# Kernel tuning notes

Hardware: AMD Instinct MI355X
Metric: run time of the kernel (lower is better)

## Reference

```python
import jax, jax.numpy as jnp
import numpy as np

B, T, D_Q, D_V, ATTN, FILTERS, KSIZE = 64, 2048, 1024, 512, 128, 32, 31


def setup_inputs() -> dict:
    key = jax.random.key(0)
    ks = jax.random.split(key, 10)
    query = jax.random.normal(ks[0], (B, D_Q), dtype=jnp.float32)
    values = jax.random.normal(ks[1], (B, T, D_V), dtype=jnp.float32)
    keys = jax.random.normal(ks[2], (B, T, ATTN), dtype=jnp.float32)
    state = jax.random.uniform(ks[3], (B, T), dtype=jnp.float32)
    # learned parameters
    W_q = jax.random.normal(ks[4], (D_Q, ATTN), dtype=jnp.float32) * 0.02
    conv_kernel = jax.random.normal(ks[5], (KSIZE, 1, FILTERS), dtype=jnp.float32) * 0.1  # (W, In, Out)
    conv_bias = jnp.zeros((FILTERS,), dtype=jnp.float32)
    W_loc = jax.random.normal(ks[6], (FILTERS, ATTN), dtype=jnp.float32) * 0.1
    v_att = jax.random.normal(ks[7], (ATTN, 1), dtype=jnp.float32) * 0.1
    att_bias = jax.random.normal(ks[8], (ATTN,), dtype=jnp.float32) * 0.02
    return {"query": query, "values": values, "keys": keys, "state": state,
            "W_q": W_q, "conv_kernel": conv_kernel, "conv_bias": conv_bias,
            "W_loc": W_loc, "v_att": v_att, "att_bias": att_bias}


def reference(query, values, keys, state, W_q, conv_kernel, conv_bias, W_loc, v_att, att_bias):
    # processed_query: [B, 1, ATTN]
    pq = (query @ W_q)[:, None, :]
    # location features: Conv1D same-padding over alignments [B, T, 1] -> [B, T, FILTERS]
    loc = jax.lax.conv_general_dilated(
        state[:, :, None], conv_kernel,
        window_strides=(1,), padding='SAME',
        dimension_numbers=('NWC', 'WIO', 'NWC')) + conv_bias
    ploc = loc @ W_loc                                  # [B, T, ATTN]
    score = jnp.tanh(keys + pq + ploc + att_bias) @ v_att  # [B, T, 1]
    alignment = jax.nn.softmax(score, axis=1)           # [B, T, 1]
    attention = jnp.sum(alignment * values, axis=1)     # [B, D_V]
    alignment = jnp.squeeze(alignment, axis=2)          # [B, T]
    attention_state = alignment + state                 # cumulate=True
    return (attention, alignment, attention_state)
```

## Files before the change

kernel.cpp:

```cpp
#include <hip/hip_runtime.h>
#include <hip/hip_bf16.h>

#define B 64
#define T 2048
#define D_Q 1024
#define D_V 512
#define ATTN 128
#define FILTERS 32
#define KSIZE 31

#define PQ_OFF 0
#define CW_OFF 8192
#define PB_OFF (8192 + 3968)
#define SC_OFF (8192 + 3968 + 128)
#define ML_OFF (SC_OFF + 131072)
#define PART_OFF (ML_OFF + 4096)

#define AT_OFF 0
#define AL_OFF 32768
#define ST_OFF (32768 + 131072)

__device__ __forceinline__ float tanh_fast(float x) {
    float e = __expf(2.f * x);
    return 1.f - 2.f / (e + 1.f);
}

__global__ void __launch_bounds__(256)
k1_precompute(const float* __restrict__ query,
              const float* __restrict__ Wq,
              const float* __restrict__ ck,
              const float* __restrict__ cbias,
              const float* __restrict__ Wl,
              const float* __restrict__ abias,
              float* __restrict__ ws) {
    int tid = threadIdx.x;
    if (blockIdx.x < B) {
        int b = blockIdx.x;
        int q = tid & 31;
        int s = tid >> 5;
        __shared__ __align__(16) float sq[D_Q];
        __shared__ float4 red[256];
        ((float4*)sq)[tid] = ((const float4*)(query + (size_t)b * D_Q))[tid];
        __syncthreads();

        const float4* Wq4 = (const float4*)Wq;
        float4 acc = make_float4(0.f, 0.f, 0.f, 0.f);
        int dbase = s << 7;
#pragma unroll 16
        for (int i = 0; i < 128; ++i) {
            int d = dbase + i;
            float sd = sq[d];
            float4 w = Wq4[(size_t)d * 32 + q];
            acc.x += sd * w.x; acc.y += sd * w.y;
            acc.z += sd * w.z; acc.w += sd * w.w;
        }
        red[tid] = acc;
        __syncthreads();
        if (tid < 128) {
            float4 o = red[tid + 128];
            acc = red[tid];
            acc.x += o.x; acc.y += o.y; acc.z += o.z; acc.w += o.w;
            red[tid] = acc;
        }
        __syncthreads();
        if (tid < 64) {
            float4 o = red[tid + 64];
            acc = red[tid];
            acc.x += o.x; acc.y += o.y; acc.z += o.z; acc.w += o.w;
            red[tid] = acc;
        }
        __syncthreads();
        if (tid < 32) {
            float4 o = red[tid + 32];
            acc = red[tid];
            acc.x += o.x; acc.y += o.y; acc.z += o.z; acc.w += o.w;
            ((float4*)(ws + PQ_OFF))[b * 32 + tid] = acc;
        }
    } else {
        __shared__ float swl[FILTERS * ATTN];
        for (int i = tid; i < FILTERS * ATTN; i += 256) swl[i] = Wl[i];
        __syncthreads();
        if (tid < ATTN) {
            int a = tid;
            for (int k = 0; k < KSIZE; ++k) {
                float acc = 0.f;
#pragma unroll
                for (int f = 0; f < FILTERS; ++f) acc += ck[k * FILTERS + f] * swl[f * ATTN + a];
                ws[CW_OFF + k * ATTN + a] = acc;
            }
            float pb = abias[a];
#pragma unroll
            for (int f = 0; f < FILTERS; ++f) pb += cbias[f] * swl[f * ATTN + a];
            ws[PB_OFF + a] = pb;
        }
    }
}

__global__ void __launch_bounds__(256)
k2_fused(const float* __restrict__ keys,
         const float* __restrict__ state,
         const float* __restrict__ values,
         const float* __restrict__ vatt,
         float* __restrict__ ws) {
    int bid = blockIdx.x;
    int b = bid >> 5;
    int c = bid & 31;
    int t0 = c << 6;
    int tid = threadIdx.x;
    int a = tid & 127;
    int h = tid >> 7;

    __shared__ __align__(16) float sstate[96];
    __shared__ float sred[128];
    __shared__ float sal[64];
    __shared__ float4 spart[128];

    if (tid < 96) {
        int idx = t0 + tid - 15;
        sstate[tid] = (idx >= 0 && idx < T) ? state[b * T + idx] : 0.f;
    }

    float cw[KSIZE];
#pragma unroll
    for (int k = 0; k < KSIZE; ++k) cw[k] = ws[CW_OFF + k * ATTN + a];
    float pqa = ws[PQ_OFF + b * ATTN + a] + ws[PB_OFF + a];
    float vat = vatt[a];

    __syncthreads();

    const float* keyrow = keys + ((size_t)b * T + t0) * ATTN + a;
    const float4* sv = (const float4*)sstate;

    for (int s4 = 0; s4 < 4; ++s4) {
        int ts = h * 32 + s4 * 8;
        float kv[8];
#pragma unroll
        for (int j = 0; j < 8; ++j) kv[j] = keyrow[(size_t)(ts + j) * ATTN];
        float w[40];
#pragma unroll
        for (int q = 0; q < 10; ++q) {
            float4 v = sv[(ts >> 2) + q];
            w[4 * q + 0] = v.x; w[4 * q + 1] = v.y;
            w[4 * q + 2] = v.z; w[4 * q + 3] = v.w;
        }
        float sc[8];
#pragma unroll
        for (int j = 0; j < 8; ++j) sc[j] = 0.f;
#pragma unroll
        for (int k = 0; k < KSIZE; ++k) {
#pragma unroll
            for (int j = 0; j < 8; ++j) sc[j] += w[j + k] * cw[k];
        }
#pragma unroll
        for (int j = 0; j < 8; ++j) {
            float x = kv[j] + pqa + sc[j];
            float cc = tanh_fast(x) * vat;
#pragma unroll
            for (int off = 32; off >= 1; off >>= 1) cc += __shfl_xor(cc, off);
            if ((tid & 63) == 0) sred[(ts + j) * 2 + (a >> 6)] = cc;
        }
    }
    __syncthreads();

    if (tid < 64) {
        float s = sred[tid * 2] + sred[tid * 2 + 1];
        ws[SC_OFF + b * T + t0 + tid] = s;
        float m = s;
#pragma unroll
        for (int off = 32; off >= 1; off >>= 1) m = fmaxf(m, __shfl_xor(m, off));
        float e = __expf(s - m);
        sal[tid] = e;
        float l = e;
#pragma unroll
        for (int off = 32; off >= 1; off >>= 1) l += __shfl_xor(l, off);
        if (tid == 0) {
            ws[ML_OFF + (b * 32 + c) * 2 + 0] = m;
            ws[ML_OFF + (b * 32 + c) * 2 + 1] = l;
        }
    }
    __syncthreads();

    int d4 = tid & 127;
    const float4* V = (const float4*)values + ((size_t)b * T + t0) * (D_V / 4) + d4;
    float4 acc = make_float4(0.f, 0.f, 0.f, 0.f);
#pragma unroll 8
    for (int i = 0; i < 32; ++i) {
        int tl = h * 32 + i;
        float al = sal[tl];
        float4 v = V[(size_t)tl * (D_V / 4)];
        acc.x += al * v.x; acc.y += al * v.y;
        acc.z += al * v.z; acc.w += al * v.w;
    }
    if (h == 1) spart[d4] = acc;
    __syncthreads();
    if (h == 0) {
        float4 o = spart[d4];
        acc.x += o.x; acc.y += o.y; acc.z += o.z; acc.w += o.w;
        ((float4*)(ws + PART_OFF))[(size_t)(b * 32 + c) * (D_V / 4) + d4] = acc;
    }
}

__global__ void __launch_bounds__(256)
k_combine(const float* __restrict__ state,
          const float* __restrict__ ws,
          float* __restrict__ out) {
    int b = blockIdx.x;
    int tid = threadIdx.x;
    __shared__ float sw[32];
    __shared__ float sM, sinvL;

    if (tid < 32) {
        float m = ws[ML_OFF + (b * 32 + tid) * 2 + 0];
        float l = ws[ML_OFF + (b * 32 + tid) * 2 + 1];
        float M = m;
#pragma unroll
        for (int off = 16; off >= 1; off >>= 1) M = fmaxf(M, __shfl_xor(M, off));
        float wgt = __expf(m - M);
        sw[tid] = wgt;
        float L = l * wgt;
#pragma unroll
        for (int off = 16; off >= 1; off >>= 1) L += __shfl_xor(L, off);
        if (tid == 0) { sM = M; sinvL = 1.f / L; }
    }
    __syncthreads();

    float M = sM, invL = sinvL;

#pragma unroll
    for (int r = 0; r < 2; ++r) {
        int d = tid + (r << 8);
        float acc = 0.f;
#pragma unroll 8
        for (int c = 0; c < 32; ++c)
            acc += sw[c] * ws[PART_OFF + (size_t)(b * 32 + c) * D_V + d];
        out[AT_OFF + b * D_V + d] = acc * invL;
    }

#pragma unroll
    for (int k = 0; k < 8; ++k) {
        int t = tid + (k << 8);
        float s = ws[SC_OFF + b * T + t];
        float al = __expf(s - M) * invL;
        out[AL_OFF + b * T + t] = al;
        out[ST_OFF + b * T + t] = al + state[b * T + t];
    }
}

extern "C" void kernel_launch(void* const* d_in, const int* in_sizes, int n_in,
                              void* d_out, int out_size, void* d_ws, size_t ws_size,
                              hipStream_t stream) {
    const float* query  = (const float*)d_in[0];
    const float* values = (const float*)d_in[1];
    const float* keys   = (const float*)d_in[2];
    const float* state  = (const float*)d_in[3];
    const float* Wq     = (const float*)d_in[4];
    const float* ck     = (const float*)d_in[5];
    const float* cbias  = (const float*)d_in[6];
    const float* Wl     = (const float*)d_in[7];
    const float* vatt   = (const float*)d_in[8];
    const float* abias  = (const float*)d_in[9];
    float* out = (float*)d_out;
    float* ws  = (float*)d_ws;

    k1_precompute<<<B + 1, 256, 0, stream>>>(query, Wq, ck, cbias, Wl, abias, ws);
    k2_fused<<<B * (T / 64), 256, 0, stream>>>(keys, state, values, vatt, ws);
    k_combine<<<B, 256, 0, stream>>>(state, ws, out);
}
```

Measured before the change: 432.7 us.

## Split fused score/value kernel into separate score and weighted-value kernels

The fused kernel is split in two. The first computes scores and per-chunk exp weights and writes the weights to workspace. The second reads those weights and does the weighted sum over values, with each half-block handling a 64-step chunk, so no shared-memory reduction is needed. The aim is to let each kernel run at better occupancy and keep register pressure from the conv path out of the value-streaming loop, at the cost of an extra launch and a workspace round trip.

```diff
diff --git a/kernel.cpp b/kernel.cpp
--- a/kernel.cpp
+++ b/kernel.cpp
@@ -15,6 +15,7 @@
 #define SC_OFF (8192 + 3968 + 128)
 #define ML_OFF (SC_OFF + 131072)
 #define PART_OFF (ML_OFF + 4096)
+#define SAL_OFF (PART_OFF + 1048576)
 
 #define AT_OFF 0
 #define AL_OFF 32768
@@ -85,7 +86,7 @@
             for (int k = 0; k < KSIZE; ++k) {
                 float acc = 0.f;
 #pragma unroll
-                for (int f = 0; f < FILTERS; ++f) acc += ck[k * FILTERS + f] * swl[f * ATTN + a];
+            for (int f = 0; f < FILTERS; ++f) acc += ck[k * FILTERS + f] * swl[f * ATTN + a];
                 ws[CW_OFF + k * ATTN + a] = acc;
             }
             float pb = abias[a];
@@ -97,11 +98,10 @@
 }
 
 __global__ void __launch_bounds__(256)
-k2_fused(const float* __restrict__ keys,
-         const float* __restrict__ state,
-         const float* __restrict__ values,
-         const float* __restrict__ vatt,
-         float* __restrict__ ws) {
+k2a_scores(const float* __restrict__ keys,
+           const float* __restrict__ state,
+           const float* __restrict__ vatt,
+           float* __restrict__ ws) {
     int bid = blockIdx.x;
     int b = bid >> 5;
     int c = bid & 31;
@@ -112,8 +112,6 @@
 
     __shared__ __align__(16) float sstate[96];
     __shared__ float sred[128];
-    __shared__ float sal[64];
-    __shared__ float4 spart[128];
 
     if (tid < 96) {
         int idx = t0 + tid - 15;
@@ -169,7 +167,7 @@
 #pragma unroll
         for (int off = 32; off >= 1; off >>= 1) m = fmaxf(m, __shfl_xor(m, off));
         float e = __expf(s - m);
-        sal[tid] = e;
+        ws[SAL_OFF + b * T + t0 + tid] = e;
         float l = e;
 #pragma unroll
         for (int off = 32; off >= 1; off >>= 1) l += __shfl_xor(l, off);
@@ -178,26 +176,36 @@
             ws[ML_OFF + (b * 32 + c) * 2 + 1] = l;
         }
     }
-    __syncthreads();
-
+}
+
+__global__ void __launch_bounds__(256)
+k2b_partial(const float* __restrict__ values,
+            float* __restrict__ ws) {
+    int bid = blockIdx.x;
+    int b = bid >> 4;
+    int cp = bid & 15;
+    int t0 = cp << 7;
+    int tid = threadIdx.x;
+    int h = tid >> 7;
     int d4 = tid & 127;
-    const float4* V = (const float4*)values + ((size_t)b * T + t0) * (D_V / 4) + d4;
+
+    __shared__ float sal[128];
+    if (tid < 128) sal[tid] = ws[SAL_OFF + b * T + t0 + tid];
+    __syncthreads();
+
+    const float4* V = (const float4*)values
+                      + ((size_t)b * T + t0 + (h << 6)) * (D_V / 4) + d4;
+    const float* wgt = sal + (h << 6);
     float4 acc = make_float4(0.f, 0.f, 0.f, 0.f);
-#pragma unroll 8
-    for (int i = 0; i < 32; ++i) {
-        int tl = h * 32 + i;
-        float al = sal[tl];
-        float4 v = V[(size_t)tl * (D_V / 4)];
+#pragma unroll 16
+    for (int i = 0; i < 64; ++i) {
+        float al = wgt[i];
+        float4 v = V[(size_t)i * (D_V / 4)];
         acc.x += al * v.x; acc.y += al * v.y;
         acc.z += al * v.z; acc.w += al * v.w;
     }
-    if (h == 1) spart[d4] = acc;
-    __syncthreads();
-    if (h == 0) {
-        float4 o = spart[d4];
-        acc.x += o.x; acc.y += o.y; acc.z += o.z; acc.w += o.w;
-        ((float4*)(ws + PART_OFF))[(size_t)(b * 32 + c) * (D_V / 4) + d4] = acc;
-    }
+    int c = (cp << 1) + h;
+    ((float4*)(ws + PART_OFF))[(size_t)(b * 32 + c) * (D_V / 4) + d4] = acc;
 }
 
 __global__ void __launch_bounds__(256)
@@ -263,6 +271,7 @@
     float* ws  = (float*)d_ws;
 
     k1_precompute<<<B + 1, 256, 0, stream>>>(query, Wq, ck, cbias, Wl, abias, ws);
-    k2_fused<<<B * (T / 64), 256, 0, stream>>>(keys, state, values, vatt, ws);
+    k2a_scores<<<B * (T / 64), 256, 0, stream>>>(keys, state, vatt, ws);
+    k2b_partial<<<B * (T / 128), 256, 0, stream>>>(values, ws);
     k_combine<<<B, 256, 0, stream>>>(state, ws, out);
 }
```

After: 443.7 us. +2.5%, slower.

## Remap score threads to float4 attention lanes, stage conv weights in LDS, split combine

Applied to the files above, without the earlier changes.

The score phase of the fused kernel is remapped so each thread owns 4 attention channels and 8 timesteps. It loads keys as float4 with nontemporal hints and reads conv-location weights from shared memory instead of 31 per-thread registers. This cuts the cross-lane shuffle reduction to a 32-lane width and lowers register pressure, with the aim of better vectorized key loads and occupancy. Values are also streamed with nontemporal loads, and the combine kernel is split four ways per batch so more blocks run in parallel.

```diff
diff --git a/kernel.cpp b/kernel.cpp
--- a/kernel.cpp
+++ b/kernel.cpp
@@ -19,6 +19,13 @@
 #define AT_OFF 0
 #define AL_OFF 32768
 #define ST_OFF (32768 + 131072)
+
+typedef float v4f __attribute__((ext_vector_type(4)));
+
+__device__ __forceinline__ float4 nt_load4(const float4* p) {
+    v4f v = __builtin_nontemporal_load((const v4f*)p);
+    return make_float4(v.x, v.y, v.z, v.w);
+}
 
 __device__ __forceinline__ float tanh_fast(float x) {
     float e = __expf(2.f * x);
@@ -107,11 +114,12 @@
     int c = bid & 31;
     int t0 = c << 6;
     int tid = threadIdx.x;
-    int a = tid & 127;
-    int h = tid >> 7;
+    int a4 = tid & 31;
+    int h = tid >> 5;
 
     __shared__ __align__(16) float sstate[96];
-    __shared__ float sred[128];
+    __shared__ __align__(16) float scw[KSIZE][ATTN];
+    __shared__ float sred[64];
     __shared__ float sal[64];
     __shared__ float4 spart[128];
 
@@ -119,51 +127,69 @@
         int idx = t0 + tid - 15;
         sstate[tid] = (idx >= 0 && idx < T) ? state[b * T + idx] : 0.f;
     }
-
-    float cw[KSIZE];
-#pragma unroll
-    for (int k = 0; k < KSIZE; ++k) cw[k] = ws[CW_OFF + k * ATTN + a];
-    float pqa = ws[PQ_OFF + b * ATTN + a] + ws[PB_OFF + a];
-    float vat = vatt[a];
-
-    __syncthreads();
-
-    const float* keyrow = keys + ((size_t)b * T + t0) * ATTN + a;
-    const float4* sv = (const float4*)sstate;
-
-    for (int s4 = 0; s4 < 4; ++s4) {
-        int ts = h * 32 + s4 * 8;
-        float kv[8];
-#pragma unroll
-        for (int j = 0; j < 8; ++j) kv[j] = keyrow[(size_t)(ts + j) * ATTN];
+    {
+        const float4* cw4 = (const float4*)(ws + CW_OFF);
+        float4* dst = (float4*)&scw[0][0];
+        for (int i = tid; i < (KSIZE * ATTN) / 4; i += 256) dst[i] = cw4[i];
+    }
+
+    float4 pq4, vat4;
+    {
+        float4 pq = ((const float4*)(ws + PQ_OFF))[b * 32 + a4];
+        float4 pb = ((const float4*)(ws + PB_OFF))[a4];
+        pq4 = make_float4(pq.x + pb.x, pq.y + pb.y, pq.z + pb.z, pq.w + pb.w);
+        vat4 = ((const float4*)vatt)[a4];
+    }
+    __syncthreads();
+
+    {
+        const float4* sv = (const float4*)sstate;
         float w[40];
+        int wq0 = h << 1;
 #pragma unroll
         for (int q = 0; q < 10; ++q) {
-            float4 v = sv[(ts >> 2) + q];
+            float4 v = sv[wq0 + q];
             w[4 * q + 0] = v.x; w[4 * q + 1] = v.y;
             w[4 * q + 2] = v.z; w[4 * q + 3] = v.w;
         }
-        float sc[8];
-#pragma unroll
-        for (int j = 0; j < 8; ++j) sc[j] = 0.f;
+
+        const float4* K4 = (const float4*)keys
+                           + ((size_t)b * T + t0 + h * 8) * (ATTN / 4) + a4;
+        float4 kv[8];
+#pragma unroll
+        for (int j = 0; j < 8; ++j)
+            kv[j] = nt_load4(&K4[(size_t)j * (ATTN / 4)]);
+
+        float4 acc[8];
+#pragma unroll
+        for (int j = 0; j < 8; ++j) acc[j] = make_float4(0.f, 0.f, 0.f, 0.f);
 #pragma unroll
         for (int k = 0; k < KSIZE; ++k) {
-#pragma unroll
-            for (int j = 0; j < 8; ++j) sc[j] += w[j + k] * cw[k];
+            float4 cwk = ((const float4*)&scw[k][0])[a4];
+#pragma unroll
+            for (int j = 0; j < 8; ++j) {
+                float wv = w[j + k];
+                acc[j].x += wv * cwk.x; acc[j].y += wv * cwk.y;
+                acc[j].z += wv * cwk.z; acc[j].w += wv * cwk.w;
+            }
         }
 #pragma unroll
         for (int j = 0; j < 8; ++j) {
-            float x = kv[j] + pqa + sc[j];
-            float cc = tanh_fast(x) * vat;
-#pragma unroll
-            for (int off = 32; off >= 1; off >>= 1) cc += __shfl_xor(cc, off);
-            if ((tid & 63) == 0) sred[(ts + j) * 2 + (a >> 6)] = cc;
+            float xx = kv[j].x + pq4.x + acc[j].x;
+            float xy = kv[j].y + pq4.y + acc[j].y;
+            float xz = kv[j].z + pq4.z + acc[j].z;
+            float xw = kv[j].w + pq4.w + acc[j].w;
+            float cc = tanh_fast(xx) * vat4.x + tanh_fast(xy) * vat4.y
+                     + tanh_fast(xz) * vat4.z + tanh_fast(xw) * vat4.w;
+#pragma unroll
+            for (int off = 16; off >= 1; off >>= 1) cc += __shfl_xor(cc, off);
+            if (a4 == 0) sred[h * 8 + j] = cc;
         }
     }
     __syncthreads();
 
     if (tid < 64) {
-        float s = sred[tid * 2] + sred[tid * 2 + 1];
+        float s = sred[tid];
         ws[SC_OFF + b * T + t0 + tid] = s;
         float m = s;
 #pragma unroll
@@ -181,19 +207,20 @@
     __syncthreads();
 
     int d4 = tid & 127;
+    int hc = tid >> 7;
     const float4* V = (const float4*)values + ((size_t)b * T + t0) * (D_V / 4) + d4;
     float4 acc = make_float4(0.f, 0.f, 0.f, 0.f);
 #pragma unroll 8
     for (int i = 0; i < 32; ++i) {
-        int tl = h * 32 + i;
+        int tl = hc * 32 + i;
         float al = sal[tl];
-        float4 v = V[(size_t)tl * (D_V / 4)];
+        float4 v = nt_load4(&V[(size_t)tl * (D_V / 4)]);
         acc.x += al * v.x; acc.y += al * v.y;
         acc.z += al * v.z; acc.w += al * v.w;
     }
-    if (h == 1) spart[d4] = acc;
-    __syncthreads();
-    if (h == 0) {
+    if (hc == 1) spart[d4] = acc;
+    __syncthreads();
+    if (hc == 0) {
         float4 o = spart[d4];
         acc.x += o.x; acc.y += o.y; acc.z += o.z; acc.w += o.w;
         ((float4*)(ws + PART_OFF))[(size_t)(b * 32 + c) * (D_V / 4) + d4] = acc;
@@ -204,7 +231,8 @@
 k_combine(const float* __restrict__ state,
           const float* __restrict__ ws,
           float* __restrict__ out) {
-    int b = blockIdx.x;
+    int b = blockIdx.x >> 2;
+    int r = blockIdx.x & 3;
     int tid = threadIdx.x;
     __shared__ float sw[32];
     __shared__ float sM, sinvL;
@@ -226,9 +254,8 @@
 
     float M = sM, invL = sinvL;
 
-#pragma unroll
-    for (int r = 0; r < 2; ++r) {
-        int d = tid + (r << 8);
+    if (tid < 128) {
+        int d = (r << 7) + tid;
         float acc = 0.f;
 #pragma unroll 8
         for (int c = 0; c < 32; ++c)
@@ -237,8 +264,8 @@
     }
 
 #pragma unroll
-    for (int k = 0; k < 8; ++k) {
-        int t = tid + (k << 8);
+    for (int k = 0; k < 2; ++k) {
+        int t = (r << 9) + tid + (k << 8);
         float s = ws[SC_OFF + b * T + t];
         float al = __expf(s - M) * invL;
         out[AL_OFF + b * T + t] = al;
@@ -264,5 +291,5 @@
 
     k1_precompute<<<B + 1, 256, 0, stream>>>(query, Wq, ck, cbias, Wl, abias, ws);
     k2_fused<<<B * (T / 64), 256, 0, stream>>>(keys, state, values, vatt, ws);
-    k_combine<<<B, 256, 0, stream>>>(state, ws, out);
-}
+    k_combine<<<B * 4, 256, 0, stream>>>(state, ws, out);
+}
```

New measurement: 417.6 us (median of 2 runs). 1.04x faster.
